# Kernel tuning notes

Measured on AMD Instinct MI355X. Metric: run time of the kernel, lower is better.

Reference implementation:

```python
import jax, jax.numpy as jnp
import numpy as np

N = 100_000   # num nodes
E = 3_200_000 # num edges (avg degree 32)
DIMS = [1, 25, 125, 125, 125, 125, 1]  # 5**2, 5**3 widths from the module


def setup_inputs() -> dict:
    key = jax.random.key(0)
    ks = jax.random.split(key, 1 + 2 * 6)
    edge_index = jax.random.randint(ks[0], (2, E), 0, N, dtype=jnp.int32)
    inp = {"edge_index": edge_index}
    for i in range(6):
        din, dout = DIMS[i], DIMS[i + 1]
        scale = jnp.sqrt(6.0 / (din + dout))  # glorot uniform
        inp[f"W{i+1}"] = jax.random.uniform(ks[1 + 2 * i], (din, dout), jnp.float32, -scale, scale)
        inp[f"b{i+1}"] = jnp.zeros((dout,), jnp.float32)
    return inp


def _gcn_layer(x, W, b, src, dst, norm):
    h = x @ W                                        # [N, dout]
    msg = h[src] * norm[:, None]                     # [E+N, dout] gather
    out = jax.ops.segment_sum(msg, dst, num_segments=N)  # scatter-add
    return out + b


def reference(edge_index, W1, b1, W2, b2, W3, b3, W4, b4, W5, b5, W6, b6):
    loop = jnp.arange(N, dtype=edge_index.dtype)
    src = jnp.concatenate([edge_index[0], loop])     # add self-loops
    dst = jnp.concatenate([edge_index[1], loop])
    deg = jax.ops.segment_sum(jnp.ones_like(src, jnp.float32), dst, num_segments=N)
    dis = jnp.where(deg > 0, jax.lax.rsqrt(jnp.maximum(deg, 1.0)), 0.0)
    norm = dis[src] * dis[dst]                       # symmetric GCN normalization

    x = jnp.ones((N, 1), jnp.float32)
    for (W, b) in ((W1, b1), (W2, b2), (W3, b3), (W4, b4), (W5, b5), (W6, b6)):
        x = _gcn_layer(x, W, b, src, dst, norm)
    # dropout is identity in eval mode; min-max normalize
    x = (x - jnp.min(x)) / (jnp.max(x) - jnp.min(x) + 1e-15)
    return x
```

## Files before the change

### kernel.cpp

```cpp
#include <hip/hip_runtime.h>
#include <hip/hip_cooperative_groups.h>

namespace cg = cooperative_groups;


#define TPB 256
#define HTPB 1024
#define NBPAD 400
#define BINE 8192
#define STAGE_CAP 12288

template <int NK, int DIN>
__device__ void coef_step8(const float* __restrict__ W, const float* __restrict__ bias,
                           const float (*in)[128], float (*out)[128],
                           float (*part)[6][128], int tid) {
    int t = tid & 127, g = tid >> 7;
    const int CH = (DIN + 7) / 8;
    int i0 = g * CH; if (i0 > DIN) i0 = DIN;
    int i1 = i0 + CH; if (i1 > DIN) i1 = DIN;
    float s[NK];
#pragma unroll
    for (int k = 0; k < NK; ++k) s[k] = 0.f;
    if (t < 125) {
#pragma unroll 4
        for (int i = i0; i < i1; ++i) {
            float w = W[i * 125 + t];
#pragma unroll
            for (int k = 0; k < NK; ++k) s[k] += w * in[k][i];
        }
    }
#pragma unroll
    for (int k = 0; k < NK; ++k) part[g][k][t] = s[k];
    __syncthreads();
    if (g == 0 && t < 125) {
#pragma unroll
        for (int k = 0; k < NK; ++k) {
            float acc = part[0][k][t];
#pragma unroll
            for (int gg = 1; gg < 8; ++gg) acc += part[gg][k][t];
            out[k + 1][t] = acc;
        }
        out[0][t] = bias[t];
    }
    __syncthreads();
}

__global__ __launch_bounds__(HTPB) void hist_coef_kernel(
    const int* __restrict__ dst, int E, int* __restrict__ bucket_cnt, int nb,
    const float* __restrict__ W1, const float* __restrict__ b1,
    const float* __restrict__ W2, const float* __restrict__ b2,
    const float* __restrict__ W3, const float* __restrict__ b3,
    const float* __restrict__ W4, const float* __restrict__ b4,
    const float* __restrict__ W5, const float* __restrict__ b5,
    const float* __restrict__ W6, const float* __restrict__ b6,
    float* __restrict__ c) {
    __shared__ int h[NBPAD];
    __shared__ float A[6][128];
    __shared__ float B[6][128];
    __shared__ float part[8][6][128];
    int tid = threadIdx.x;
    int nbh = gridDim.x - 1;

    if ((int)blockIdx.x < nbh) {
        for (int j = tid; j < NBPAD; j += HTPB) h[j] = 0;
        __syncthreads();
        const int E4 = E >> 2;
        const int chunk4 = (E4 + nbh - 1) / nbh;
        const int b4 = (int)blockIdx.x * chunk4;
        const int e4 = (b4 + chunk4 < E4) ? (b4 + chunk4) : E4;
        const int4* d4 = (const int4*)dst;
        for (int j = b4 + tid; j < e4; j += HTPB) {
            int4 v = d4[j];
            atomicAdd(&h[v.x >> 8], 1);
            atomicAdd(&h[v.y >> 8], 1);
            atomicAdd(&h[v.z >> 8], 1);
            atomicAdd(&h[v.w >> 8], 1);
        }
        if (blockIdx.x == 0) {
            for (int j = (E4 << 2) + tid; j < E; j += HTPB) atomicAdd(&h[dst[j] >> 8], 1);
        }
        __syncthreads();
        for (int j = tid; j < nb; j += HTPB)
            if (h[j]) atomicAdd(&bucket_cnt[j], h[j]);
        return;
    }

    if (tid < 25) { A[1][tid] = W1[tid]; A[0][tid] = b1[tid]; }
    __syncthreads();
    coef_step8<2, 25>(W2, b2, A, B, part, tid);
    coef_step8<3, 125>(W3, b3, B, A, part, tid);
    coef_step8<4, 125>(W4, b4, A, B, part, tid);
    coef_step8<5, 125>(W5, b5, B, A, part, tid);
    int wave = tid >> 6, lane = tid & 63;
    if (wave < 6) {
        int k = wave;
        float acc = (lane < 125 ? W6[lane] * A[k][lane] : 0.f)
                  + (lane + 64 < 125 ? W6[lane + 64] * A[k][lane + 64] : 0.f);
        for (int off = 32; off > 0; off >>= 1) acc += __shfl_down(acc, off);
        if (lane == 0) c[k + 1] = acc;
    }
    if (tid == 0) c[0] = b6[0];
}

__global__ void bucket_scan(const int* __restrict__ bucket_cnt, int nb,
                            int* __restrict__ bucket_base, int* __restrict__ bucket_cursor,
                            int* __restrict__ rowptr, int n, int E) {
    __shared__ int s[512];
    int t = threadIdx.x;
    int v = (t < nb) ? bucket_cnt[t] : 0;
    s[t] = v;
    __syncthreads();
    for (int off = 1; off < 512; off <<= 1) {
        int a = (t >= off) ? s[t - off] : 0;
        __syncthreads();
        s[t] += a;
        __syncthreads();
    }
    if (t < nb) {
        int ex = s[t] - v;
        bucket_base[t] = ex;
        bucket_cursor[t] = ex;
    }
    if (t == 0) { bucket_base[nb] = E; rowptr[n] = E; }
}

__global__ __launch_bounds__(256) void binA_kernel(
    const int* __restrict__ src, const int* __restrict__ dst, int E,
    int* __restrict__ bucket_cursor, unsigned int* __restrict__ binned) {
    __shared__ int cnt[NBPAD];
    __shared__ int sa[512], sb[512];
    __shared__ int lbase[NBPAD];
    __shared__ int gbase[NBPAD];
    __shared__ int lcur[NBPAD];
    __shared__ unsigned int stagew[BINE];
    __shared__ unsigned short sbuck[BINE];
    int t = threadIdx.x;
    long long base = (long long)blockIdx.x * BINE;
    int ne = (E - base < BINE) ? (int)(E - base) : BINE;

    for (int j = t; j < NBPAD; j += 256) cnt[j] = 0;
    __syncthreads();

    int dv[8][4];
    const int4* d4 = (const int4*)(dst + base);
#pragma unroll
    for (int i = 0; i < 8; ++i) {
        int j4 = t + i * 256;
        if ((j4 << 2) + 3 < ne) {
            int4 v = d4[j4];
            dv[i][0] = v.x; dv[i][1] = v.y; dv[i][2] = v.z; dv[i][3] = v.w;
        } else {
#pragma unroll
            for (int cx = 0; cx < 4; ++cx) {
                int j = (j4 << 2) + cx;
                dv[i][cx] = (j < ne) ? dst[base + j] : -1;
            }
        }
#pragma unroll
        for (int cx = 0; cx < 4; ++cx)
            if (dv[i][cx] >= 0) atomicAdd(&cnt[dv[i][cx] >> 8], 1);
    }
    __syncthreads();
    for (int j = t; j < 512; j += 256) sa[j] = (j < NBPAD) ? cnt[j] : 0;
    __syncthreads();
    int* cu = sa; int* nx = sb;
    for (int off = 1; off < 512; off <<= 1) {
        for (int j = t; j < 512; j += 256) nx[j] = cu[j] + (j >= off ? cu[j - off] : 0);
        __syncthreads();
        int* tmp = cu; cu = nx; nx = tmp;
    }
    for (int j = t; j < NBPAD; j += 256) {
        int ex = cu[j] - cnt[j];
        lbase[j] = ex;
        lcur[j] = ex;
        gbase[j] = cnt[j] ? atomicAdd(&bucket_cursor[j], cnt[j]) : 0;
    }
    __syncthreads();
    const int4* s4 = (const int4*)(src + base);
#pragma unroll
    for (int i = 0; i < 8; ++i) {
        int j4 = t + i * 256;
        int sv[4];
        if ((j4 << 2) + 3 < ne) {
            int4 v = s4[j4];
            sv[0] = v.x; sv[1] = v.y; sv[2] = v.z; sv[3] = v.w;
        } else {
#pragma unroll
            for (int cx = 0; cx < 4; ++cx) {
                int j = (j4 << 2) + cx;
                sv[cx] = (j < ne) ? src[base + j] : -1;
            }
        }
#pragma unroll
        for (int cx = 0; cx < 4; ++cx) {
            if (dv[i][cx] >= 0) {
                int bk = dv[i][cx] >> 8;
                int pos = atomicAdd(&lcur[bk], 1);
                stagew[pos] = ((unsigned)(dv[i][cx] & 255) << 24) | (unsigned)sv[cx];
                sbuck[pos] = (unsigned short)bk;
            }
        }
    }
    __syncthreads();
    for (int j = t; j < ne; j += 256) {
        int bk = sbuck[j];
        binned[gbase[bk] + (j - lbase[bk])] = stagew[j];
    }
}

__global__ __launch_bounds__(256) void csrB_kernel(
    const unsigned int* __restrict__ binned,
    const int* __restrict__ bucket_base, int n,
    int* __restrict__ rowptr, int* __restrict__ csr, float* __restrict__ dis) {
    __shared__ int deg[256];
    __shared__ int ex[256];
    __shared__ int cur[256];
    __shared__ int stage[STAGE_CAP];
    int b = blockIdx.x;
    int t = threadIdx.x;
    int ebase = bucket_base[b], eend = bucket_base[b + 1];
    int esize = eend - ebase;
    int gnode = (b << 8) + t;
    deg[t] = 0;
    __syncthreads();
    int a0 = (ebase + 3) & ~3; if (a0 > eend) a0 = eend;
    int a1 = eend & ~3;        if (a1 < a0) a1 = a0;
    for (int e = ebase + t; e < a0; e += 256) atomicAdd(&deg[binned[e] >> 24], 1);
    {
        const uint4* b4 = (const uint4*)(binned + a0);
        int n4 = (a1 - a0) >> 2;
        for (int j = t; j < n4; j += 256) {
            uint4 v = b4[j];
            atomicAdd(&deg[v.x >> 24], 1);
            atomicAdd(&deg[v.y >> 24], 1);
            atomicAdd(&deg[v.z >> 24], 1);
            atomicAdd(&deg[v.w >> 24], 1);
        }
    }
    for (int e = a1 + t; e < eend; e += 256) atomicAdd(&deg[binned[e] >> 24], 1);
    __syncthreads();
    int d = deg[t];
    ex[t] = d;
    __syncthreads();
    for (int off = 1; off < 256; off <<= 1) {
        int a = (t >= off) ? ex[t - off] : 0;
        __syncthreads();
        ex[t] += a;
        __syncthreads();
    }
    int excl = ex[t] - d;
    if (gnode < n) {
        rowptr[gnode] = ebase + excl;
        dis[gnode] = rsqrtf((float)d + 1.0f);
    }
    cur[t] = excl;
    __syncthreads();
    if (esize <= STAGE_CAP) {
        for (int e = ebase + t; e < a0; e += 256) {
            unsigned int pk = binned[e];
            stage[atomicAdd(&cur[pk >> 24], 1)] = (int)(pk & 0xffffffu);
        }
        {
            const uint4* b4 = (const uint4*)(binned + a0);
            int n4 = (a1 - a0) >> 2;
            for (int j = t; j < n4; j += 256) {
                uint4 v = b4[j];
                stage[atomicAdd(&cur[v.x >> 24], 1)] = (int)(v.x & 0xffffffu);
                stage[atomicAdd(&cur[v.y >> 24], 1)] = (int)(v.y & 0xffffffu);
                stage[atomicAdd(&cur[v.z >> 24], 1)] = (int)(v.z & 0xffffffu);
                stage[atomicAdd(&cur[v.w >> 24], 1)] = (int)(v.w & 0xffffffu);
            }
        }
        for (int e = a1 + t; e < eend; e += 256) {
            unsigned int pk = binned[e];
            stage[atomicAdd(&cur[pk >> 24], 1)] = (int)(pk & 0xffffffu);
        }
        __syncthreads();
        for (int e = t; e < esize; e += 256) csr[ebase + e] = stage[e];
    } else {
        for (int e = ebase + t; e < eend; e += 256) {
            unsigned int pk = binned[e];
            int pos = atomicAdd(&cur[pk >> 24], 1);
            csr[ebase + pos] = (int)(pk & 0xffffffu);
        }
    }
}

template <int NS, int CBT>
__global__ __launch_bounds__(256, 8) void coop_gather_t(
    const int* __restrict__ rowptr, const int* __restrict__ csr,
    const float* __restrict__ dis, float* __restrict__ qA, float* __restrict__ qB,
    const float* __restrict__ c,
    float* __restrict__ bmin, float* __restrict__ bmax,
    float* __restrict__ out, int n) {
    cg::grid_group grid = cg::this_grid();
    __shared__ float smn[256], smx[256];
    int t = threadIdx.x;
    int lane = t & 15, grp = t >> 4;
    int gid0 = (int)blockIdx.x * 16 + grp;

    int beg[NS], end[NS];
    float dd[NS], qown[NS], vacc[NS];
    float cc[7];
#pragma unroll
    for (int k = 0; k < 7; ++k) cc[k] = c[k];

#pragma unroll
    for (int s = 0; s < NS; ++s) {
        int node = gid0 + s * (CBT * 16);
        bool act = node < n;
        beg[s] = act ? rowptr[node] : 0;
        end[s] = act ? rowptr[node + 1] : 0;
        dd[s]  = act ? dis[node] : 0.f;
        qown[s] = dd[s];
        vacc[s] = cc[0];
    }

    const float* q = dis;
    for (int k = 1; k <= 6; ++k) {
        float* qn = (k & 1) ? qA : qB;
#pragma unroll
        for (int s = 0; s < NS; ++s) {
            float acc = 0.f;
            for (int e = beg[s] + lane; e < end[s]; e += 16)
                acc += q[csr[e]];
#pragma unroll
            for (int off = 8; off > 0; off >>= 1) acc += __shfl_down(acc, off, 16);
            int node = gid0 + s * (CBT * 16);
            if (lane == 0 && node < n) {
                float p = dd[s] * (acc + qown[s]);
                qown[s] = dd[s] * p;
                if (k < 6) qn[node] = qown[s];
                vacc[s] += cc[k] * p;
            }
        }
        if (k < 6) {
            __threadfence();
            grid.sync();
            q = qn;
        }
    }

    float mn = 1e30f, mx = -1e30f;
    if (lane == 0) {
#pragma unroll
        for (int s = 0; s < NS; ++s) {
            int node = gid0 + s * (CBT * 16);
            if (node < n) { mn = fminf(mn, vacc[s]); mx = fmaxf(mx, vacc[s]); }
        }
    }
    smn[t] = mn; smx[t] = mx;
    __syncthreads();
    for (int sft = 128; sft > 0; sft >>= 1) {
        if (t < sft) {
            smn[t] = fminf(smn[t], smn[t + sft]);
            smx[t] = fmaxf(smx[t], smx[t + sft]);
        }
        __syncthreads();
    }
    if (t == 0) { bmin[blockIdx.x] = smn[0]; bmax[blockIdx.x] = smx[0]; }
    __threadfence();
    grid.sync();

    mn = 1e30f; mx = -1e30f;
    for (int j = t; j < CBT; j += 256) {
        mn = fminf(mn, bmin[j]);
        mx = fmaxf(mx, bmax[j]);
    }
    smn[t] = mn; smx[t] = mx;
    __syncthreads();
    for (int sft = 128; sft > 0; sft >>= 1) {
        if (t < sft) {
            smn[t] = fminf(smn[t], smn[t + sft]);
            smx[t] = fmaxf(smx[t], smx[t + sft]);
        }
        __syncthreads();
    }
    mn = smn[0]; mx = smx[0];
    float inv = 1.0f / (mx - mn + 1e-15f);
    if (lane == 0) {
#pragma unroll
        for (int s = 0; s < NS; ++s) {
            int node = gid0 + s * (CBT * 16);
            if (node < n) out[node] = (vacc[s] - mn) * inv;
        }
    }
}

__global__ void gather_step(const int* __restrict__ rowptr, const int* __restrict__ csr,
                            const float* __restrict__ dis, const float* __restrict__ q,
                            const float* __restrict__ c, int k,
                            float* __restrict__ qnext, float* __restrict__ vacc,
                            int n, int first) {
    int tid = blockIdx.x * blockDim.x + threadIdx.x;
    int node = tid >> 4;
    int lane = tid & 15;
    if (node >= n) return;
    int beg = rowptr[node], end = rowptr[node + 1];
    float acc = 0.f;
    for (int e = beg + lane; e < end; e += 16) acc += q[csr[e]];
    for (int off = 8; off > 0; off >>= 1) acc += __shfl_down(acc, off, 16);
    if (lane == 0) {
        float d = dis[node];
        float p = d * (acc + q[node]);
        qnext[node] = d * p;
        float add = c[k] * p;
        vacc[node] = first ? (c[0] + add) : (vacc[node] + add);
    }
}

__global__ void gather_last(const int* __restrict__ rowptr, const int* __restrict__ csr,
                            const float* __restrict__ dis, const float* __restrict__ q,
                            const float* __restrict__ c,
                            float* __restrict__ vacc,
                            float* __restrict__ bmin, float* __restrict__ bmax, int n) {
    __shared__ float smn[TPB], smx[TPB];
    int t = threadIdx.x;
    int tid = blockIdx.x * blockDim.x + t;
    int node = tid >> 4;
    int lane = tid & 15;
    float v = 1e30f;
    bool act = (node < n);
    if (act) {
        int beg = rowptr[node], end = rowptr[node + 1];
        float acc = 0.f;
        for (int e = beg + lane; e < end; e += 16) acc += q[csr[e]];
        for (int off = 8; off > 0; off >>= 1) acc += __shfl_down(acc, off, 16);
        if (lane == 0) {
            float d = dis[node];
            float p = d * (acc + q[node]);
            v = vacc[node] + c[6] * p;
            vacc[node] = v;
        }
    }
    smn[t] = (act && lane == 0) ? v : 1e30f;
    smx[t] = (act && lane == 0) ? v : -1e30f;
    __syncthreads();
    for (int s = TPB / 2; s > 0; s >>= 1) {
        if (t < s) { smn[t] = fminf(smn[t], smn[t + s]); smx[t] = fmaxf(smx[t], smx[t + s]); }
        __syncthreads();
    }
    if (t == 0) { bmin[blockIdx.x] = smn[0]; bmax[blockIdx.x] = smx[0]; }
}

__global__ void minmax_final_kernel(const float* __restrict__ bmin, const float* __restrict__ bmax,
                                    int nblk, float* __restrict__ mnmx) {
    __shared__ float smn[TPB], smx[TPB];
    int t = threadIdx.x;
    float mn = 1e30f, mx = -1e30f;
    for (int i = t; i < nblk; i += TPB) {
        mn = fminf(mn, bmin[i]);
        mx = fmaxf(mx, bmax[i]);
    }
    smn[t] = mn; smx[t] = mx;
    __syncthreads();
    for (int s = TPB / 2; s > 0; s >>= 1) {
        if (t < s) { smn[t] = fminf(smn[t], smn[t + s]); smx[t] = fmaxf(smx[t], smx[t + s]); }
        __syncthreads();
    }
    if (t == 0) { mnmx[0] = smn[0]; mnmx[1] = smx[0]; }
}

__global__ void normalize_kernel(const float* __restrict__ v, const float* __restrict__ mnmx,
                                 float* __restrict__ out, int n) {
    int i = blockIdx.x * blockDim.x + threadIdx.x;
    if (i < n) {
        float mn = mnmx[0], mx = mnmx[1];
        out[i] = (v[i] - mn) / (mx - mn + 1e-15f);
    }
}

static inline int cdiv(long long a, int b) { return (int)((a + b - 1) / b); }

extern "C" void kernel_launch(void* const* d_in, const int* in_sizes, int n_in,
                              void* d_out, int out_size, void* d_ws, size_t ws_size,
                              hipStream_t stream) {
    const int N = out_size;
    const int E = in_sizes[0] / 2;
    const int* src = (const int*)d_in[0];
    const int* dst = src + E;

    const float* W1 = (const float*)d_in[1];  const float* b1 = (const float*)d_in[2];
    const float* W2 = (const float*)d_in[3];  const float* b2 = (const float*)d_in[4];
    const float* W3 = (const float*)d_in[5];  const float* b3 = (const float*)d_in[6];
    const float* W4 = (const float*)d_in[7];  const float* b4 = (const float*)d_in[8];
    const float* W5 = (const float*)d_in[9];  const float* b5 = (const float*)d_in[10];
    const float* W6 = (const float*)d_in[11]; const float* b6 = (const float*)d_in[12];

    const int nb = (N + 255) >> 8;
    const int gblocks = cdiv((long long)N * 16, TPB);

    char* p = (char*)d_ws;
    int*   bucket_cnt    = (int*)p;   p += (size_t)512 * 4;
    int*   bucket_base   = (int*)p;   p += (size_t)512 * 4;
    int*   bucket_cursor = (int*)p;   p += (size_t)512 * 4;
    int*   rowptr        = (int*)p;   p += (size_t)(N + 1) * 4;
    int*   csr           = (int*)p;   p += (size_t)E * 4;
    unsigned int* binned = (unsigned int*)p; p += (size_t)E * 4;
    float* dis    = (float*)p; p += (size_t)N * 4;
    float* qA     = (float*)p; p += (size_t)N * 4;
    float* qB     = (float*)p; p += (size_t)N * 4;
    float* vacc   = (float*)p; p += (size_t)N * 4;
    float* c      = (float*)p; p += (size_t)8 * 4;
    float* bmin   = (float*)p; p += (size_t)gblocks * 4;
    float* bmax   = (float*)p; p += (size_t)gblocks * 4;
    float* mnmx   = (float*)p; p += 2 * 4;

    hipMemsetAsync(bucket_cnt, 0, 512 * 4, stream);
    const int nbh = 128;
    hist_coef_kernel<<<nbh + 1, HTPB, 0, stream>>>(dst, E, bucket_cnt, nb,
                                                   W1, b1, W2, b2, W3, b3,
                                                   W4, b4, W5, b5, W6, b6, c);
    bucket_scan<<<1, 512, 0, stream>>>(bucket_cnt, nb, bucket_base, bucket_cursor,
                                       rowptr, N, E);
    binA_kernel<<<cdiv(E, BINE), 256, 0, stream>>>(src, dst, E, bucket_cursor, binned);
    csrB_kernel<<<nb, 256, 0, stream>>>(binned, bucket_base, N, rowptr, csr, dis);

    constexpr int CB8 = 2048, NS8 = 4;
    int occ = 0;
    hipError_t oerr = hipOccupancyMaxActiveBlocksPerMultiprocessor(
        &occ, (const void*)coop_gather_t<NS8, CB8>, 256, 0);
    bool canCoop = (oerr == hipSuccess) && ((long long)occ * 256 >= CB8) &&
                   (N <= CB8 * 16 * NS8);
    if (canCoop) {
        const int* rp = rowptr; const int* cs = csr;
        const float* dis_c = dis; const float* cc = c;
        float* qA_ = qA; float* qB_ = qB;
        float* bmin_ = bmin; float* bmax_ = bmax;
        float* outp = (float*)d_out;
        int n_ = N;
        void* args[] = { &rp, &cs, &dis_c, &qA_, &qB_, &cc, &bmin_, &bmax_, &outp, &n_ };
        hipLaunchCooperativeKernel((const void*)coop_gather_t<NS8, CB8>,
                                   dim3(CB8), dim3(256), args, 0, stream);
    } else {
        gather_step<<<gblocks, TPB, 0, stream>>>(rowptr, csr, dis, dis, c, 1, qA, vacc, N, 1);
        gather_step<<<gblocks, TPB, 0, stream>>>(rowptr, csr, dis, qA,  c, 2, qB, vacc, N, 0);
        gather_step<<<gblocks, TPB, 0, stream>>>(rowptr, csr, dis, qB,  c, 3, qA, vacc, N, 0);
        gather_step<<<gblocks, TPB, 0, stream>>>(rowptr, csr, dis, qA,  c, 4, qB, vacc, N, 0);
        gather_step<<<gblocks, TPB, 0, stream>>>(rowptr, csr, dis, qB,  c, 5, qA, vacc, N, 0);
        gather_last<<<gblocks, TPB, 0, stream>>>(rowptr, csr, dis, qA, c, vacc, bmin, bmax, N);
        minmax_final_kernel<<<1, TPB, 0, stream>>>(bmin, bmax, gblocks, mnmx);
        normalize_kernel<<<cdiv(N, TPB), TPB, 0, stream>>>(vacc, mnmx, (float*)d_out, N);
    }
}
```

Measured before the change: 173.0 us.

## Replace histogram+scan pass with fixed-capacity buckets and overflow list

Drops the separate destination histogram pass and bucket scan. Each bucket now gets a fixed-capacity slot region (CAP entries), and a global overflow list catches excess edges. CSR rows are described by rowptr/rowend pairs instead of a dense prefix, and the coefficient computation moves into an extra block of the binning kernel, which now runs with 1024 threads. This removes one full read of dst and two kernel launches. In exchange it uses a larger workspace, and every csrB block scans the whole overflow list, which becomes costly if overflow is large.

```diff
diff --git a/kernel.cpp b/kernel.cpp
--- a/kernel.cpp
+++ b/kernel.cpp
@@ -5,10 +5,18 @@
 
 
 #define TPB 256
-#define HTPB 1024
 #define NBPAD 400
 #define BINE 8192
+#define CAP 9216
 #define STAGE_CAP 12288
+#define BATPB 1024
+
+__global__ void init_kernel(int* __restrict__ cursor, int nb,
+                            int* __restrict__ ovf_cnt, int* __restrict__ csr_ovf_cur) {
+    int t = blockIdx.x * blockDim.x + threadIdx.x;
+    if (t < nb) cursor[t] = t * CAP;
+    if (t == nb) { ovf_cnt[0] = 0; csr_ovf_cur[0] = 0; }
+}
 
 template <int NK, int DIN>
 __device__ void coef_step8(const float* __restrict__ W, const float* __restrict__ bias,
@@ -45,8 +53,25 @@
     __syncthreads();
 }
 
-__global__ __launch_bounds__(HTPB) void hist_coef_kernel(
-    const int* __restrict__ dst, int E, int* __restrict__ bucket_cnt, int nb,
+struct BinSh {
+    int cnt[NBPAD];
+    int sa[512], sb[512];
+    int lbase[NBPAD], gbase[NBPAD], lcur[NBPAD];
+    unsigned int stagew[BINE];
+    unsigned short sbuck[BINE];
+};
+struct CoefSh {
+    float A[6][128];
+    float B[6][128];
+    float part[8][6][128];
+};
+union BinAU { BinSh a; CoefSh cs; };
+
+__global__ __launch_bounds__(BATPB) void binA_kernel(
+    const int* __restrict__ src, const int* __restrict__ dst, int E,
+    int* __restrict__ cursor, unsigned int* __restrict__ binned,
+    unsigned int* __restrict__ ovf_w, unsigned short* __restrict__ ovf_b,
+    int* __restrict__ ovf_cnt,
     const float* __restrict__ W1, const float* __restrict__ b1,
     const float* __restrict__ W2, const float* __restrict__ b2,
     const float* __restrict__ W3, const float* __restrict__ b3,
@@ -54,98 +79,40 @@
     const float* __restrict__ W5, const float* __restrict__ b5,
     const float* __restrict__ W6, const float* __restrict__ b6,
     float* __restrict__ c) {
-    __shared__ int h[NBPAD];
-    __shared__ float A[6][128];
-    __shared__ float B[6][128];
-    __shared__ float part[8][6][128];
-    int tid = threadIdx.x;
-    int nbh = gridDim.x - 1;
-
-    if ((int)blockIdx.x < nbh) {
-        for (int j = tid; j < NBPAD; j += HTPB) h[j] = 0;
-        __syncthreads();
-        const int E4 = E >> 2;
-        const int chunk4 = (E4 + nbh - 1) / nbh;
-        const int b4 = (int)blockIdx.x * chunk4;
-        const int e4 = (b4 + chunk4 < E4) ? (b4 + chunk4) : E4;
-        const int4* d4 = (const int4*)dst;
-        for (int j = b4 + tid; j < e4; j += HTPB) {
-            int4 v = d4[j];
-            atomicAdd(&h[v.x >> 8], 1);
-            atomicAdd(&h[v.y >> 8], 1);
-            atomicAdd(&h[v.z >> 8], 1);
-            atomicAdd(&h[v.w >> 8], 1);
-        }
-        if (blockIdx.x == 0) {
-            for (int j = (E4 << 2) + tid; j < E; j += HTPB) atomicAdd(&h[dst[j] >> 8], 1);
-        }
-        __syncthreads();
-        for (int j = tid; j < nb; j += HTPB)
-            if (h[j]) atomicAdd(&bucket_cnt[j], h[j]);
+    __shared__ BinAU u;
+    int t = threadIdx.x;
+    int nbA = gridDim.x - 1;
+
+    if ((int)blockIdx.x >= nbA) {
+        if (t < 25) { u.cs.A[1][t] = W1[t]; u.cs.A[0][t] = b1[t]; }
+        __syncthreads();
+        coef_step8<2, 25>(W2, b2, u.cs.A, u.cs.B, u.cs.part, t);
+        coef_step8<3, 125>(W3, b3, u.cs.B, u.cs.A, u.cs.part, t);
+        coef_step8<4, 125>(W4, b4, u.cs.A, u.cs.B, u.cs.part, t);
+        coef_step8<5, 125>(W5, b5, u.cs.B, u.cs.A, u.cs.part, t);
+        int wave = t >> 6, lane = t & 63;
+        if (wave < 6) {
+            int k = wave;
+            float acc = (lane < 125 ? W6[lane] * u.cs.A[k][lane] : 0.f)
+                      + (lane + 64 < 125 ? W6[lane + 64] * u.cs.A[k][lane + 64] : 0.f);
+            for (int off = 32; off > 0; off >>= 1) acc += __shfl_down(acc, off);
+            if (lane == 0) c[k + 1] = acc;
+        }
+        if (t == 0) c[0] = b6[0];
         return;
     }
 
-    if (tid < 25) { A[1][tid] = W1[tid]; A[0][tid] = b1[tid]; }
-    __syncthreads();
-    coef_step8<2, 25>(W2, b2, A, B, part, tid);
-    coef_step8<3, 125>(W3, b3, B, A, part, tid);
-    coef_step8<4, 125>(W4, b4, A, B, part, tid);
-    coef_step8<5, 125>(W5, b5, B, A, part, tid);
-    int wave = tid >> 6, lane = tid & 63;
-    if (wave < 6) {
-        int k = wave;
-        float acc = (lane < 125 ? W6[lane] * A[k][lane] : 0.f)
-                  + (lane + 64 < 125 ? W6[lane + 64] * A[k][lane + 64] : 0.f);
-        for (int off = 32; off > 0; off >>= 1) acc += __shfl_down(acc, off);
-        if (lane == 0) c[k + 1] = acc;
-    }
-    if (tid == 0) c[0] = b6[0];
-}
-
-__global__ void bucket_scan(const int* __restrict__ bucket_cnt, int nb,
-                            int* __restrict__ bucket_base, int* __restrict__ bucket_cursor,
-                            int* __restrict__ rowptr, int n, int E) {
-    __shared__ int s[512];
-    int t = threadIdx.x;
-    int v = (t < nb) ? bucket_cnt[t] : 0;
-    s[t] = v;
-    __syncthreads();
-    for (int off = 1; off < 512; off <<= 1) {
-        int a = (t >= off) ? s[t - off] : 0;
-        __syncthreads();
-        s[t] += a;
-        __syncthreads();
-    }
-    if (t < nb) {
-        int ex = s[t] - v;
-        bucket_base[t] = ex;
-        bucket_cursor[t] = ex;
-    }
-    if (t == 0) { bucket_base[nb] = E; rowptr[n] = E; }
-}
-
-__global__ __launch_bounds__(256) void binA_kernel(
-    const int* __restrict__ src, const int* __restrict__ dst, int E,
-    int* __restrict__ bucket_cursor, unsigned int* __restrict__ binned) {
-    __shared__ int cnt[NBPAD];
-    __shared__ int sa[512], sb[512];
-    __shared__ int lbase[NBPAD];
-    __shared__ int gbase[NBPAD];
-    __shared__ int lcur[NBPAD];
-    __shared__ unsigned int stagew[BINE];
-    __shared__ unsigned short sbuck[BINE];
-    int t = threadIdx.x;
     long long base = (long long)blockIdx.x * BINE;
     int ne = (E - base < BINE) ? (int)(E - base) : BINE;
 
-    for (int j = t; j < NBPAD; j += 256) cnt[j] = 0;
-    __syncthreads();
-
-    int dv[8][4];
+    for (int j = t; j < NBPAD; j += BATPB) u.a.cnt[j] = 0;
+    __syncthreads();
+
+    int dv[2][4];
     const int4* d4 = (const int4*)(dst + base);
 #pragma unroll
-    for (int i = 0; i < 8; ++i) {
-        int j4 = t + i * 256;
+    for (int i = 0; i < 2; ++i) {
+        int j4 = t + i * BATPB;
         if ((j4 << 2) + 3 < ne) {
             int4 v = d4[j4];
             dv[i][0] = v.x; dv[i][1] = v.y; dv[i][2] = v.z; dv[i][3] = v.w;
@@ -158,28 +125,28 @@
         }
 #pragma unroll
         for (int cx = 0; cx < 4; ++cx)
-            if (dv[i][cx] >= 0) atomicAdd(&cnt[dv[i][cx] >> 8], 1);
-    }
-    __syncthreads();
-    for (int j = t; j < 512; j += 256) sa[j] = (j < NBPAD) ? cnt[j] : 0;
-    __syncthreads();
-    int* cu = sa; int* nx = sb;
+            if (dv[i][cx] >= 0) atomicAdd(&u.a.cnt[dv[i][cx] >> 8], 1);
+    }
+    __syncthreads();
+    for (int j = t; j < 512; j += BATPB) u.a.sa[j] = (j < NBPAD) ? u.a.cnt[j] : 0;
+    __syncthreads();
+    int* cu = u.a.sa; int* nx = u.a.sb;
     for (int off = 1; off < 512; off <<= 1) {
-        for (int j = t; j < 512; j += 256) nx[j] = cu[j] + (j >= off ? cu[j - off] : 0);
+        for (int j = t; j < 512; j += BATPB) nx[j] = cu[j] + (j >= off ? cu[j - off] : 0);
         __syncthreads();
         int* tmp = cu; cu = nx; nx = tmp;
     }
-    for (int j = t; j < NBPAD; j += 256) {
-        int ex = cu[j] - cnt[j];
-        lbase[j] = ex;
-        lcur[j] = ex;
-        gbase[j] = cnt[j] ? atomicAdd(&bucket_cursor[j], cnt[j]) : 0;
+    for (int j = t; j < NBPAD; j += BATPB) {
+        int ex = cu[j] - u.a.cnt[j];
+        u.a.lbase[j] = ex;
+        u.a.lcur[j] = ex;
+        u.a.gbase[j] = u.a.cnt[j] ? atomicAdd(&cursor[j], u.a.cnt[j]) : 0;
     }
     __syncthreads();
     const int4* s4 = (const int4*)(src + base);
 #pragma unroll
-    for (int i = 0; i < 8; ++i) {
-        int j4 = t + i * 256;
+    for (int i = 0; i < 2; ++i) {
+        int j4 = t + i * BATPB;
         int sv[4];
         if ((j4 << 2) + 3 < ne) {
             int4 v = s4[j4];
@@ -195,40 +162,52 @@
         for (int cx = 0; cx < 4; ++cx) {
             if (dv[i][cx] >= 0) {
                 int bk = dv[i][cx] >> 8;
-                int pos = atomicAdd(&lcur[bk], 1);
-                stagew[pos] = ((unsigned)(dv[i][cx] & 255) << 24) | (unsigned)sv[cx];
-                sbuck[pos] = (unsigned short)bk;
-            }
-        }
-    }
-    __syncthreads();
-    for (int j = t; j < ne; j += 256) {
-        int bk = sbuck[j];
-        binned[gbase[bk] + (j - lbase[bk])] = stagew[j];
+                int pos = atomicAdd(&u.a.lcur[bk], 1);
+                u.a.stagew[pos] = ((unsigned)(dv[i][cx] & 255) << 24) | (unsigned)sv[cx];
+                u.a.sbuck[pos] = (unsigned short)bk;
+            }
+        }
+    }
+    __syncthreads();
+    for (int j = t; j < ne; j += BATPB) {
+        int bk = u.a.sbuck[j];
+        int pos = u.a.gbase[bk] + (j - u.a.lbase[bk]);
+        if (pos < (bk + 1) * CAP) {
+            binned[pos] = u.a.stagew[j];
+        } else {
+            int ov = atomicAdd(ovf_cnt, 1);
+            ovf_w[ov] = u.a.stagew[j];
+            ovf_b[ov] = (unsigned short)bk;
+        }
     }
 }
 
 __global__ __launch_bounds__(256) void csrB_kernel(
-    const unsigned int* __restrict__ binned,
-    const int* __restrict__ bucket_base, int n,
-    int* __restrict__ rowptr, int* __restrict__ csr, float* __restrict__ dis) {
+    const unsigned int* __restrict__ binned, const int* __restrict__ cursor,
+    const unsigned int* __restrict__ ovf_w, const unsigned short* __restrict__ ovf_b,
+    const int* __restrict__ ovf_cnt, int* __restrict__ csr_ovf_cur,
+    int nb, int n,
+    int* __restrict__ rowptr, int* __restrict__ rowend,
+    int* __restrict__ csr, float* __restrict__ dis) {
     __shared__ int deg[256];
     __shared__ int ex[256];
     __shared__ int cur[256];
     __shared__ int stage[STAGE_CAP];
+    __shared__ int sh_obase;
     int b = blockIdx.x;
     int t = threadIdx.x;
-    int ebase = bucket_base[b], eend = bucket_base[b + 1];
-    int esize = eend - ebase;
+    int ebase = b * CAP;
+    int total = cursor[b] - ebase;
+    int mainsz = total < CAP ? total : CAP;
+    int eend = ebase + mainsz;
+    int ovfn = ovf_cnt[0];
     int gnode = (b << 8) + t;
     deg[t] = 0;
     __syncthreads();
-    int a0 = (ebase + 3) & ~3; if (a0 > eend) a0 = eend;
-    int a1 = eend & ~3;        if (a1 < a0) a1 = a0;
-    for (int e = ebase + t; e < a0; e += 256) atomicAdd(&deg[binned[e] >> 24], 1);
     {
-        const uint4* b4 = (const uint4*)(binned + a0);
-        int n4 = (a1 - a0) >> 2;
+        int a1 = ebase + (mainsz & ~3);
+        const uint4* b4 = (const uint4*)(binned + ebase);
+        int n4 = (a1 - ebase) >> 2;
         for (int j = t; j < n4; j += 256) {
             uint4 v = b4[j];
             atomicAdd(&deg[v.x >> 24], 1);
@@ -236,8 +215,10 @@
             atomicAdd(&deg[v.z >> 24], 1);
             atomicAdd(&deg[v.w >> 24], 1);
         }
-    }
-    for (int e = a1 + t; e < eend; e += 256) atomicAdd(&deg[binned[e] >> 24], 1);
+        for (int e = a1 + t; e < eend; e += 256) atomicAdd(&deg[binned[e] >> 24], 1);
+    }
+    for (int i = t; i < ovfn; i += 256)
+        if (ovf_b[i] == b) atomicAdd(&deg[ovf_w[i] >> 24], 1);
     __syncthreads();
     int d = deg[t];
     ex[t] = d;
@@ -249,20 +230,24 @@
         __syncthreads();
     }
     int excl = ex[t] - d;
+    if (t == 0) {
+        if (total <= CAP) sh_obase = ebase;
+        else sh_obase = nb * CAP + atomicAdd(csr_ovf_cur, total);
+    }
+    __syncthreads();
+    int obase = sh_obase;
     if (gnode < n) {
-        rowptr[gnode] = ebase + excl;
+        rowptr[gnode] = obase + excl;
+        rowend[gnode] = obase + excl + d;
         dis[gnode] = rsqrtf((float)d + 1.0f);
     }
     cur[t] = excl;
     __syncthreads();
-    if (esize <= STAGE_CAP) {
-        for (int e = ebase + t; e < a0; e += 256) {
-            unsigned int pk = binned[e];
-            stage[atomicAdd(&cur[pk >> 24], 1)] = (int)(pk & 0xffffffu);
-        }
+    if (total <= STAGE_CAP) {
         {
-            const uint4* b4 = (const uint4*)(binned + a0);
-            int n4 = (a1 - a0) >> 2;
+            int a1 = ebase + (mainsz & ~3);
+            const uint4* b4 = (const uint4*)(binned + ebase);
+            int n4 = (a1 - ebase) >> 2;
             for (int j = t; j < n4; j += 256) {
                 uint4 v = b4[j];
                 stage[atomicAdd(&cur[v.x >> 24], 1)] = (int)(v.x & 0xffffffu);
@@ -270,25 +255,39 @@
                 stage[atomicAdd(&cur[v.z >> 24], 1)] = (int)(v.z & 0xffffffu);
                 stage[atomicAdd(&cur[v.w >> 24], 1)] = (int)(v.w & 0xffffffu);
             }
-        }
-        for (int e = a1 + t; e < eend; e += 256) {
-            unsigned int pk = binned[e];
-            stage[atomicAdd(&cur[pk >> 24], 1)] = (int)(pk & 0xffffffu);
-        }
-        __syncthreads();
-        for (int e = t; e < esize; e += 256) csr[ebase + e] = stage[e];
+            for (int e = a1 + t; e < eend; e += 256) {
+                unsigned int pk = binned[e];
+                stage[atomicAdd(&cur[pk >> 24], 1)] = (int)(pk & 0xffffffu);
+            }
+        }
+        for (int i = t; i < ovfn; i += 256) {
+            if (ovf_b[i] == b) {
+                unsigned int pk = ovf_w[i];
+                stage[atomicAdd(&cur[pk >> 24], 1)] = (int)(pk & 0xffffffu);
+            }
+        }
+        __syncthreads();
+        for (int e = t; e < total; e += 256) csr[obase + e] = stage[e];
     } else {
         for (int e = ebase + t; e < eend; e += 256) {
             unsigned int pk = binned[e];
             int pos = atomicAdd(&cur[pk >> 24], 1);
-            csr[ebase + pos] = (int)(pk & 0xffffffu);
+            csr[obase + pos] = (int)(pk & 0xffffffu);
+        }
+        for (int i = t; i < ovfn; i += 256) {
+            if (ovf_b[i] == b) {
+                unsigned int pk = ovf_w[i];
+                int pos = atomicAdd(&cur[pk >> 24], 1);
+                csr[obase + pos] = (int)(pk & 0xffffffu);
+            }
         }
     }
 }
 
 template <int NS, int CBT>
 __global__ __launch_bounds__(256, 8) void coop_gather_t(
-    const int* __restrict__ rowptr, const int* __restrict__ csr,
+    const int* __restrict__ rowptr, const int* __restrict__ rowend,
+    const int* __restrict__ csr,
     const float* __restrict__ dis, float* __restrict__ qA, float* __restrict__ qB,
     const float* __restrict__ c,
     float* __restrict__ bmin, float* __restrict__ bmax,
@@ -310,7 +309,7 @@
         int node = gid0 + s * (CBT * 16);
         bool act = node < n;
         beg[s] = act ? rowptr[node] : 0;
-        end[s] = act ? rowptr[node + 1] : 0;
+        end[s] = act ? rowend[node] : 0;
         dd[s]  = act ? dis[node] : 0.f;
         qown[s] = dd[s];
         vacc[s] = cc[0];
@@ -387,7 +386,8 @@
     }
 }
 
-__global__ void gather_step(const int* __restrict__ rowptr, const int* __restrict__ csr,
+__global__ void gather_step(const int* __restrict__ rowptr, const int* __restrict__ rowend,
+                            const int* __restrict__ csr,
                             const float* __restrict__ dis, const float* __restrict__ q,
                             const float* __restrict__ c, int k,
                             float* __restrict__ qnext, float* __restrict__ vacc,
@@ -396,7 +396,7 @@
     int node = tid >> 4;
     int lane = tid & 15;
     if (node >= n) return;
-    int beg = rowptr[node], end = rowptr[node + 1];
+    int beg = rowptr[node], end = rowend[node];
     float acc = 0.f;
     for (int e = beg + lane; e < end; e += 16) acc += q[csr[e]];
     for (int off = 8; off > 0; off >>= 1) acc += __shfl_down(acc, off, 16);
@@ -409,7 +409,8 @@
     }
 }
 
-__global__ void gather_last(const int* __restrict__ rowptr, const int* __restrict__ csr,
+__global__ void gather_last(const int* __restrict__ rowptr, const int* __restrict__ rowend,
+                            const int* __restrict__ csr,
                             const float* __restrict__ dis, const float* __restrict__ q,
                             const float* __restrict__ c,
                             float* __restrict__ vacc,
@@ -422,7 +423,7 @@
     float v = 1e30f;
     bool act = (node < n);
     if (act) {
-        int beg = rowptr[node], end = rowptr[node + 1];
+        int beg = rowptr[node], end = rowend[node];
         float acc = 0.f;
         for (int e = beg + lane; e < end; e += 16) acc += q[csr[e]];
         for (int off = 8; off > 0; off >>= 1) acc += __shfl_down(acc, off, 16);
@@ -489,32 +490,36 @@
 
     const int nb = (N + 255) >> 8;
     const int gblocks = cdiv((long long)N * 16, TPB);
+    const size_t nbCAP = (size_t)nb * CAP;
 
     char* p = (char*)d_ws;
-    int*   bucket_cnt    = (int*)p;   p += (size_t)512 * 4;
-    int*   bucket_base   = (int*)p;   p += (size_t)512 * 4;
-    int*   bucket_cursor = (int*)p;   p += (size_t)512 * 4;
-    int*   rowptr        = (int*)p;   p += (size_t)(N + 1) * 4;
-    int*   csr           = (int*)p;   p += (size_t)E * 4;
-    unsigned int* binned = (unsigned int*)p; p += (size_t)E * 4;
+    unsigned int* binned = (unsigned int*)p; p += nbCAP * 4;
+    int*   csr           = (int*)p;          p += (nbCAP + (size_t)E) * 4;
+    unsigned int* ovf_w  = (unsigned int*)p; p += (size_t)E * 4;
+    int*   rowptr        = (int*)p;          p += (size_t)N * 4;
+    int*   rowend        = (int*)p;          p += (size_t)N * 4;
     float* dis    = (float*)p; p += (size_t)N * 4;
     float* qA     = (float*)p; p += (size_t)N * 4;
     float* qB     = (float*)p; p += (size_t)N * 4;
     float* vacc   = (float*)p; p += (size_t)N * 4;
-    float* c      = (float*)p; p += (size_t)8 * 4;
     float* bmin   = (float*)p; p += (size_t)gblocks * 4;
     float* bmax   = (float*)p; p += (size_t)gblocks * 4;
+    float* c      = (float*)p; p += (size_t)8 * 4;
     float* mnmx   = (float*)p; p += 2 * 4;
-
-    hipMemsetAsync(bucket_cnt, 0, 512 * 4, stream);
-    const int nbh = 128;
-    hist_coef_kernel<<<nbh + 1, HTPB, 0, stream>>>(dst, E, bucket_cnt, nb,
-                                                   W1, b1, W2, b2, W3, b3,
-                                                   W4, b4, W5, b5, W6, b6, c);
-    bucket_scan<<<1, 512, 0, stream>>>(bucket_cnt, nb, bucket_base, bucket_cursor,
-                                       rowptr, N, E);
-    binA_kernel<<<cdiv(E, BINE), 256, 0, stream>>>(src, dst, E, bucket_cursor, binned);
-    csrB_kernel<<<nb, 256, 0, stream>>>(binned, bucket_base, N, rowptr, csr, dis);
+    int*   cursor = (int*)p;   p += (size_t)512 * 4;
+    int*   ovf_cnt = (int*)p;  p += 4;
+    int*   csr_ovf_cur = (int*)p; p += 4;
+    unsigned short* ovf_b = (unsigned short*)p; p += (size_t)E * 2;
+
+    init_kernel<<<2, 256, 0, stream>>>(cursor, nb, ovf_cnt, csr_ovf_cur);
+    const int nbA = cdiv(E, BINE);
+    binA_kernel<<<nbA + 1, BATPB, 0, stream>>>(src, dst, E, cursor, binned,
+                                               ovf_w, ovf_b, ovf_cnt,
+                                               W1, b1, W2, b2, W3, b3,
+                                               W4, b4, W5, b5, W6, b6, c);
+    csrB_kernel<<<nb, 256, 0, stream>>>(binned, cursor, ovf_w, ovf_b, ovf_cnt,
+                                        csr_ovf_cur, nb, N,
+                                        rowptr, rowend, csr, dis);
 
     constexpr int CB8 = 2048, NS8 = 4;
     int occ = 0;
@@ -523,22 +528,23 @@
     bool canCoop = (oerr == hipSuccess) && ((long long)occ * 256 >= CB8) &&
                    (N <= CB8 * 16 * NS8);
     if (canCoop) {
-        const int* rp = rowptr; const int* cs = csr;
+        const int* rp = rowptr; const int* re = rowend; const int* cs = csr;
         const float* dis_c = dis; const float* cc = c;
         float* qA_ = qA; float* qB_ = qB;
         float* bmin_ = bmin; float* bmax_ = bmax;
         float* outp = (float*)d_out;
         int n_ = N;
-        void* args[] = { &rp, &cs, &dis_c, &qA_, &qB_, &cc, &bmin_, &bmax_, &outp, &n_ };
+        void* args[] = { &rp, &re, &cs, &dis_c, &qA_, &qB_, &cc,
+                         &bmin_, &bmax_, &outp, &n_ };
         hipLaunchCooperativeKernel((const void*)coop_gather_t<NS8, CB8>,
                                    dim3(CB8), dim3(256), args, 0, stream);
     } else {
-        gather_step<<<gblocks, TPB, 0, stream>>>(rowptr, csr, dis, dis, c, 1, qA, vacc, N, 1);
-        gather_step<<<gblocks, TPB, 0, stream>>>(rowptr, csr, dis, qA,  c, 2, qB, vacc, N, 0);
-        gather_step<<<gblocks, TPB, 0, stream>>>(rowptr, csr, dis, qB,  c, 3, qA, vacc, N, 0);
-        gather_step<<<gblocks, TPB, 0, stream>>>(rowptr, csr, dis, qA,  c, 4, qB, vacc, N, 0);
-        gather_step<<<gblocks, TPB, 0, stream>>>(rowptr, csr, dis, qB,  c, 5, qA, vacc, N, 0);
-        gather_last<<<gblocks, TPB, 0, stream>>>(rowptr, csr, dis, qA, c, vacc, bmin, bmax, N);
+        gather_step<<<gblocks, TPB, 0, stream>>>(rowptr, rowend, csr, dis, dis, c, 1, qA, vacc, N, 1);
+        gather_step<<<gblocks, TPB, 0, stream>>>(rowptr, rowend, csr, dis, qA,  c, 2, qB, vacc, N, 0);
+        gather_step<<<gblocks, TPB, 0, stream>>>(rowptr, rowend, csr, dis, qB,  c, 3, qA, vacc, N, 0);
+        gather_step<<<gblocks, TPB, 0, stream>>>(rowptr, rowend, csr, dis, qA,  c, 4, qB, vacc, N, 0);
+        gather_step<<<gblocks, TPB, 0, stream>>>(rowptr, rowend, csr, dis, qB,  c, 5, qA, vacc, N, 0);
+        gather_last<<<gblocks, TPB, 0, stream>>>(rowptr, rowend, csr, dis, qA, c, vacc, bmin, bmax, N);
         minmax_final_kernel<<<1, TPB, 0, stream>>>(bmin, bmax, gblocks, mnmx);
         normalize_kernel<<<cdiv(N, TPB), TPB, 0, stream>>>(vacc, mnmx, (float*)d_out, N);
     }
```

Measured after the change: 156.8 us. -9.4%, faster.
